# Performance work log

Measured on AMD Instinct MI355X. Metric: run time of the kernel, lower is better.

## Reference

```python
import jax, jax.numpy as jnp
import numpy as np

N, E, IN, OUT, EF = 20000, 100000, 32, 32, 16
NEG = -1e30  # finite sentinel for masked scores (avoids inf*0 grads)


def setup_inputs() -> dict:
    key = jax.random.key(0)
    ks = jax.random.split(key, 8)
    return {
        "feat": jax.random.normal(ks[0], (N, IN), jnp.float32),
        "efeat": jax.random.normal(ks[1], (E, EF), jnp.float32),
        "src": jax.random.randint(ks[2], (E,), 0, N, dtype=jnp.int32),
        "dst": jax.random.randint(ks[3], (E,), 0, N, dtype=jnp.int32),
        "etype": jax.random.randint(ks[4], (E,), 0, 2, dtype=jnp.int32),
        "attn_w": jax.random.normal(ks[5], (2 * IN, 1), jnp.float32) * 0.1,
        "attn_b": jnp.zeros((1,), jnp.float32),
        "ef1_w": jax.random.normal(ks[6], (EF, IN * OUT), jnp.float32) * 0.05,
        "ef1_b": jnp.zeros((IN * OUT,), jnp.float32),
        "ef2_w": jax.random.normal(ks[7], (EF, IN * OUT), jnp.float32) * 0.05,
        "ef2_b": jnp.zeros((IN * OUT,), jnp.float32),
        "bias": jnp.zeros((OUT,), jnp.float32),
    }


def reference(feat, efeat, src, dst, etype, attn_w, attn_b,
              ef1_w, ef1_b, ef2_w, ef2_b, bias):
    n_nodes = feat.shape[0]
    z_src = feat[src]                      # [E, IN] gather src features
    z_dst = feat[dst]                      # [E, IN] gather dst features
    # per-edge scalar attention score: leaky_relu(Linear(cat(z_src, z_dst)))
    score = jax.nn.leaky_relu(
        (jnp.concatenate([z_src, z_dst], axis=1) @ attn_w + attn_b)[:, 0]
    )  # [E]

    def relation_agg(mask, w, b):
        # edge-specific weight matrices: [E, IN, OUT]
        We = (efeat @ w + b).reshape(E, IN, OUT)
        # message per edge = src_feat @ W_e  (sum over IN commutes with attn)
        msg = jnp.einsum('ei,eio->eo', z_src, We)        # [E, OUT]
        # segment softmax over incoming edges of this relation per dst node
        s = jnp.where(mask, score, NEG)
        smax = jax.ops.segment_max(s, dst, num_segments=n_nodes)
        ex = jnp.where(mask, jnp.exp(s - smax[dst]), 0.0)
        den = jax.ops.segment_sum(ex, dst, num_segments=n_nodes)
        alpha = ex / jnp.where(den > 0, den, 1.0)[dst]   # [E]
        # attention-weighted scatter-sum to dst nodes
        return jax.ops.segment_sum(alpha[:, None] * msg, dst,
                                   num_segments=n_nodes)  # [N, OUT]

    rst = relation_agg(etype == 0, ef1_w, ef1_b) \
        + relation_agg(etype == 1, ef2_w, ef2_b) \
        + bias
    return rst
```

## Files before the change

### kernel.cpp

```cpp
#include <hip/hip_runtime.h>

typedef __attribute__((ext_vector_type(8))) short bf16x8;
typedef __attribute__((ext_vector_type(16))) float f32x16;
typedef __attribute__((ext_vector_type(2))) float f32x2;

__device__ __forceinline__ unsigned short f2b(float x) {
    unsigned u = __float_as_uint(x);
    unsigned r = (u + 0x7fffu + ((u >> 16) & 1u)) >> 16;
    return (unsigned short)r;
}
__device__ __forceinline__ unsigned f2b2(float lo, float hi) {
    return (unsigned)f2b(lo) | ((unsigned)f2b(hi) << 16);
}
__device__ __forceinline__ float b2f(unsigned short u) {
    return __uint_as_float((unsigned)u << 16);
}
__device__ __forceinline__ f32x2 pk_fma(f32x2 a, f32x2 b, f32x2 c) {
    f32x2 d;
    asm("v_pk_fma_f32 %0, %1, %2, %3" : "=v"(d) : "v"(a), "v"(b), "v"(c));
    return d;
}

__global__ void k_zero(int* __restrict__ histden, int* __restrict__ lkb,
                       const float* __restrict__ feat, const float* __restrict__ attn_w,
                       const float* __restrict__ w1, const float* __restrict__ b1,
                       const float* __restrict__ w2, const float* __restrict__ b2,
                       float* __restrict__ ps, float* __restrict__ pd,
                       unsigned short* __restrict__ PA, int N) {
    int idx = blockIdx.x * blockDim.x + threadIdx.x;
    int n4q = N;
    if (idx < n4q) ((int4*)histden)[idx] = make_int4(0, 0, 0, 0);
    if (idx < 16) ((int4*)lkb)[idx] = make_int4(0, 0, 0, 0);
    if (idx < N) {
        const float4* zp = (const float4*)(feat + (long)idx * 32);
        const float4* aw = (const float4*)attn_w;
        float a = 0.f, b = 0.f;
        #pragma unroll
        for (int j = 0; j < 8; ++j) {
            float4 z = zp[j], wa = aw[j], wb = aw[8 + j];
            a = fmaf(z.x, wa.x, a); a = fmaf(z.y, wa.y, a);
            a = fmaf(z.z, wa.z, a); a = fmaf(z.w, wa.w, a);
            b = fmaf(z.x, wb.x, b); b = fmaf(z.y, wb.y, b);
            b = fmaf(z.z, wb.z, b); b = fmaf(z.w, wb.w, b);
        }
        ps[idx] = a; pd[idx] = b;
    }
    if (idx < 2 * 17 * 2 * 64) {
        int l = idx & 63;
        int x = idx >> 6;
        int h = x & 1; x >>= 1;
        int t = x % 17;
        int r = x / 17;
        const float* W = r ? w2 : w1;
        const float* B = r ? b2 : b1;
        int o = l & 31;
        int kb = h * 16 + (l >> 5) * 8;
        unsigned short v[8];
        #pragma unroll
        for (int j = 0; j < 8; ++j) {
            int i = kb + j;
            float sv = (t < 16) ? W[t * 1024 + i * 32 + o] : B[i * 32 + o];
            v[j] = f2b(sv);
        }
        uint4 pack;
        pack.x = (unsigned)v[0] | ((unsigned)v[1] << 16);
        pack.y = (unsigned)v[2] | ((unsigned)v[3] << 16);
        pack.z = (unsigned)v[4] | ((unsigned)v[5] << 16);
        pack.w = (unsigned)v[6] | ((unsigned)v[7] << 16);
        *((uint4*)PA + idx) = pack;
    }
}

__global__ void k_hist(const int* __restrict__ dst, const int* __restrict__ etype,
                       int* __restrict__ hist, int E, int N) {
    int e = blockIdx.x * blockDim.x + threadIdx.x;
    if (e < E) atomicAdd(&hist[etype[e] * N + dst[e]], 1);
}

__global__ __launch_bounds__(256) void k_scan(const int* __restrict__ hist,
                                              int* __restrict__ rowptr,
                                              int* __restrict__ cursor,
                                              int* __restrict__ lkb, int n, int E) {
    __shared__ int s[256];
    __shared__ int soff;
    int t = threadIdx.x, b = blockIdx.x;
    int i0 = b * 1024 + t * 4;
    int4 hv = make_int4(0, 0, 0, 0);
    if (i0 + 3 < n) hv = *(const int4*)(hist + i0);
    else {
        if (i0 + 0 < n) hv.x = hist[i0 + 0];
        if (i0 + 1 < n) hv.y = hist[i0 + 1];
        if (i0 + 2 < n) hv.z = hist[i0 + 2];
        if (i0 + 3 < n) hv.w = hist[i0 + 3];
    }
    int tot = hv.x + hv.y + hv.z + hv.w;
    s[t] = tot;
    __syncthreads();
    for (int d = 1; d < 256; d <<= 1) {
        int x = (t >= d) ? s[t - d] : 0;
        __syncthreads();
        s[t] += x;
        __syncthreads();
    }
    if (t == 255) atomicExch(&lkb[b], s[255] + 1);
    if (t < 64) {
        int v = 0;
        if (t < b) {
            int p;
            do { p = atomicAdd(&lkb[t], 0); } while (p == 0);
            v = p - 1;
        }
        #pragma unroll
        for (int d = 32; d >= 1; d >>= 1) v += __shfl_down(v, d);
        if (t == 0) soff = v;
    }
    __syncthreads();
    int run = s[t] - tot + soff;
    if (i0 + 0 < n) { rowptr[i0 + 0] = run; cursor[i0 + 0] = run; } run += hv.x;
    if (i0 + 1 < n) { rowptr[i0 + 1] = run; cursor[i0 + 1] = run; } run += hv.y;
    if (i0 + 2 < n) { rowptr[i0 + 2] = run; cursor[i0 + 2] = run; } run += hv.z;
    if (i0 + 3 < n) { rowptr[i0 + 3] = run; cursor[i0 + 3] = run; }
    if (t == 0 && b == 0) rowptr[n] = E;
}

__global__ void k_score(const int* __restrict__ src, const int* __restrict__ dst,
                        const int* __restrict__ etype,
                        const float* __restrict__ ps, const float* __restrict__ pd,
                        const float* __restrict__ attn_b,
                        int* __restrict__ cursor, float* __restrict__ den,
                        int* __restrict__ sortidx, float* __restrict__ exs,
                        int E, int N) {
    int e = blockIdx.x * blockDim.x + threadIdx.x;
    if (e >= E) return;
    int d = dst[e];
    float sc = ps[src[e]] + pd[d] + attn_b[0];
    sc = sc >= 0.f ? sc : 0.01f * sc;
    float v = __expf(sc);
    int key = etype[e] * N + d;
    atomicAdd(&den[key], v);
    int pos = atomicAdd(&cursor[key], 1);
    sortidx[pos] = e;
    exs[pos] = v;
}

__global__ __launch_bounds__(256) void k_msg(
    const float* __restrict__ feat, const float* __restrict__ efeat,
    const int* __restrict__ src, const unsigned short* __restrict__ PA,
    const int* __restrict__ sortidx, const int* __restrict__ rowptr,
    unsigned short* __restrict__ wmsg, int E, int N) {
    int r = blockIdx.y;
    int cnt0 = rowptr[N];
    int relstart = r ? cnt0 : 0;
    int count = r ? (E - cnt0) : cnt0;
    int base = blockIdx.x * 128;
    if (count <= 0 || base >= count) return;

    __shared__ __align__(16) char smem[18432];
    unsigned short (*z_bf)[32] = (unsigned short(*)[32])smem;
    float (*ut)[128] = (float(*)[128])(smem + 8192);
    float (*msgl)[36] = (float(*)[36])smem;

    int tid = threadIdx.x;
    {
        int el = tid >> 1, half = tid & 1;
        int gi = base + el;
        int e = sortidx[relstart + min(gi, count - 1)];
        int sn = src[e];
        const float4* zp = (const float4*)(feat + (long)sn * 32 + half * 16);
        float4 a0 = zp[0], a1 = zp[1], a2 = zp[2], a3 = zp[3];
        uint4 p0, p1;
        p0.x = f2b2(a0.x, a0.y); p0.y = f2b2(a0.z, a0.w);
        p0.z = f2b2(a1.x, a1.y); p0.w = f2b2(a1.z, a1.w);
        p1.x = f2b2(a2.x, a2.y); p1.y = f2b2(a2.z, a2.w);
        p1.z = f2b2(a3.x, a3.y); p1.w = f2b2(a3.z, a3.w);
        uint4* zd = (uint4*)&z_bf[el][half * 16];
        zd[0] = p0; zd[1] = p1;
        const float4* up = (const float4*)(efeat + (long)e * 16 + half * 8);
        float4 c0 = up[0], c1 = up[1];
        int fb = half * 8;
        ut[fb + 0][el] = c0.x; ut[fb + 1][el] = c0.y;
        ut[fb + 2][el] = c0.z; ut[fb + 3][el] = c0.w;
        ut[fb + 4][el] = c1.x; ut[fb + 5][el] = c1.y;
        ut[fb + 6][el] = c1.z; ut[fb + 7][el] = c1.w;
    }
    __syncthreads();

    int lane = tid & 63;
    int ecol = (tid >> 6) * 32 + (lane & 31);
    int kb = (lane >> 5) * 8;
    bf16x8 b0 = *(const bf16x8*)&z_bf[ecol][kb];
    bf16x8 b1 = *(const bf16x8*)&z_bf[ecol][16 + kb];

    float uu[16];
    #pragma unroll
    for (int t = 0; t < 16; ++t) uu[t] = ut[t][ecol];

    const bf16x8* pa = (const bf16x8*)PA + (long)r * 34 * 64 + lane;

    f32x2 m2[8];
    {
        bf16x8 a0 = pa[32 * 64];
        bf16x8 a1 = pa[33 * 64];
        f32x16 c;
        #pragma unroll
        for (int k = 0; k < 16; ++k) c[k] = 0.f;
        c = __builtin_amdgcn_mfma_f32_32x32x16_bf16(a0, b0, c, 0, 0, 0);
        c = __builtin_amdgcn_mfma_f32_32x32x16_bf16(a1, b1, c, 0, 0, 0);
        #pragma unroll
        for (int k = 0; k < 8; ++k) { m2[k][0] = c[2 * k]; m2[k][1] = c[2 * k + 1]; }
    }
    #pragma unroll 4
    for (int t = 0; t < 16; ++t) {
        bf16x8 a0 = pa[(t * 2 + 0) * 64];
        bf16x8 a1 = pa[(t * 2 + 1) * 64];
        f32x16 c;
        #pragma unroll
        for (int k = 0; k < 16; ++k) c[k] = 0.f;
        c = __builtin_amdgcn_mfma_f32_32x32x16_bf16(a0, b0, c, 0, 0, 0);
        c = __builtin_amdgcn_mfma_f32_32x32x16_bf16(a1, b1, c, 0, 0, 0);
        f32x2 ud; ud[0] = uu[t]; ud[1] = uu[t];
        #pragma unroll
        for (int k = 0; k < 8; ++k) {
            f32x2 cc; cc[0] = c[2 * k]; cc[1] = c[2 * k + 1];
            m2[k] = pk_fma(ud, cc, m2[k]);
        }
    }
    __syncthreads();

    {
        int ob = 4 * (lane >> 5);
        float4* mq = (float4*)&msgl[ecol][ob];
        mq[0] = make_float4(m2[0][0], m2[0][1], m2[1][0], m2[1][1]);
        mq[2] = make_float4(m2[2][0], m2[2][1], m2[3][0], m2[3][1]);
        mq[4] = make_float4(m2[4][0], m2[4][1], m2[5][0], m2[5][1]);
        mq[6] = make_float4(m2[6][0], m2[6][1], m2[7][0], m2[7][1]);
    }
    __syncthreads();

    {
        uint4* wb = (uint4*)(wmsg + (long)(relstart + base) * 32);
        #pragma unroll
        for (int j = 0; j < 2; ++j) {
            int flat = j * 256 + tid;
            int row = flat >> 2, col = (flat & 3) * 8;
            if (base + row < count) {
                const float* mr = &msgl[row][col];
                uint4 pk;
                pk.x = f2b2(mr[0], mr[1]);
                pk.y = f2b2(mr[2], mr[3]);
                pk.z = f2b2(mr[4], mr[5]);
                pk.w = f2b2(mr[6], mr[7]);
                wb[flat] = pk;
            }
        }
    }
}

__global__ void k_reduce(const int* __restrict__ rowptr, const float* __restrict__ exs,
                         const float* __restrict__ den,
                         const unsigned short* __restrict__ wmsg,
                         const float* __restrict__ bias,
                         float* __restrict__ out, int N) {
    int tid = blockIdx.x * blockDim.x + threadIdx.x;
    if (tid >= N * 8) return;
    int n = tid >> 3, og = tid & 7;
    float4 acc = ((const float4*)bias)[og];
    #pragma unroll 1
    for (int r = 0; r < 2; ++r) {
        int k = r * N + n;
        int s = rowptr[k], e2 = rowptr[k + 1];
        if (s >= e2) continue;
        float inv = 1.f / den[k];
        #pragma unroll 1
        for (int p = s; p < e2; ++p) {
            float w = exs[p] * inv;
            ushort4 m = *(const ushort4*)(wmsg + (long)p * 32 + og * 4);
            acc.x = fmaf(w, b2f(m.x), acc.x);
            acc.y = fmaf(w, b2f(m.y), acc.y);
            acc.z = fmaf(w, b2f(m.z), acc.z);
            acc.w = fmaf(w, b2f(m.w), acc.w);
        }
    }
    ((float4*)out)[tid] = acc;
}

extern "C" void kernel_launch(void* const* d_in, const int* in_sizes, int n_in,
                              void* d_out, int out_size, void* d_ws, size_t ws_size,
                              hipStream_t stream) {
    const float* feat   = (const float*)d_in[0];
    const float* efeat  = (const float*)d_in[1];
    const int*   src    = (const int*)d_in[2];
    const int*   dst    = (const int*)d_in[3];
    const int*   etype  = (const int*)d_in[4];
    const float* attn_w = (const float*)d_in[5];
    const float* attn_b = (const float*)d_in[6];
    const float* ef1_w  = (const float*)d_in[7];
    const float* ef1_b  = (const float*)d_in[8];
    const float* ef2_w  = (const float*)d_in[9];
    const float* ef2_b  = (const float*)d_in[10];
    const float* bias   = (const float*)d_in[11];

    int E = in_sizes[2];
    int N = in_sizes[0] / 32;
    int n2 = 2 * N;
    int nb = (n2 + 1023) / 1024;

    float*          ps      = (float*)d_ws;
    float*          pd      = ps + N;
    unsigned short* PA      = (unsigned short*)(pd + N);
    int*            hist    = (int*)(PA + 2 * 17 * 2 * 64 * 8);
    float*          den     = (float*)(hist + n2);
    int*            rowptr  = (int*)(den + n2);
    int*            cursor  = rowptr + n2 + 1;
    int*            lkb     = cursor + n2;
    int*            sortidx = lkb + 64;
    float*          exs     = (float*)(sortidx + E);
    unsigned short* wmsg    = (unsigned short*)(((size_t)(exs + E) + 15) & ~(size_t)15);
    float*          out     = (float*)d_out;

    k_zero<<<(N + 255) / 256, 256, 0, stream>>>(hist, lkb, feat, attn_w,
                                                ef1_w, ef1_b, ef2_w, ef2_b,
                                                ps, pd, PA, N);
    k_hist<<<(E + 255) / 256, 256, 0, stream>>>(dst, etype, hist, E, N);
    k_scan<<<nb, 256, 0, stream>>>(hist, rowptr, cursor, lkb, n2, E);
    k_score<<<(E + 255) / 256, 256, 0, stream>>>(src, dst, etype, ps, pd, attn_b,
                                                 cursor, den, sortidx, exs, E, N);
    dim3 mgrid((E + 127) / 128, 2);
    k_msg<<<mgrid, 256, 0, stream>>>(feat, efeat, src, PA, sortidx, rowptr,
                                     wmsg, E, N);
    k_reduce<<<(N * 8 + 255) / 256, 256, 0, stream>>>(rowptr, exs, den, wmsg, bias, out, N);
}
```

Measured before the change: 52.98 us.

## Drop denominator atomics and LDS staging in message kernel

Removes the per-edge atomicAdd into the softmax denominator array. Instead, k_reduce sums the sorted exp values over each CSR segment before normalising, which costs an extra pass over exs per node. k_msg now loads each edge's source features and edge features directly into registers in MFMA operand layout and writes bf16 messages straight to global memory. This drops the LDS staging, the transposes and the three barriers, at the cost of redundant per-lane global loads and narrower, less coalesced stores. Zeroing now covers only the histogram, since the den buffer is gone.

```diff
diff --git a/kernel.cpp b/kernel.cpp
--- a/kernel.cpp
+++ b/kernel.cpp
@@ -21,15 +21,15 @@
     return d;
 }
 
-__global__ void k_zero(int* __restrict__ histden, int* __restrict__ lkb,
+__global__ void k_zero(int* __restrict__ hist, int* __restrict__ lkb,
                        const float* __restrict__ feat, const float* __restrict__ attn_w,
                        const float* __restrict__ w1, const float* __restrict__ b1,
                        const float* __restrict__ w2, const float* __restrict__ b2,
                        float* __restrict__ ps, float* __restrict__ pd,
                        unsigned short* __restrict__ PA, int N) {
     int idx = blockIdx.x * blockDim.x + threadIdx.x;
-    int n4q = N;
-    if (idx < n4q) ((int4*)histden)[idx] = make_int4(0, 0, 0, 0);
+    int n2q = (2 * N + 3) >> 2;
+    if (idx < n2q) ((int4*)hist)[idx] = make_int4(0, 0, 0, 0);
     if (idx < 16) ((int4*)lkb)[idx] = make_int4(0, 0, 0, 0);
     if (idx < N) {
         const float4* zp = (const float4*)(feat + (long)idx * 32);
@@ -127,9 +127,8 @@
                         const int* __restrict__ etype,
                         const float* __restrict__ ps, const float* __restrict__ pd,
                         const float* __restrict__ attn_b,
-                        int* __restrict__ cursor, float* __restrict__ den,
-                        int* __restrict__ sortidx, float* __restrict__ exs,
-                        int E, int N) {
+                        int* __restrict__ cursor, int* __restrict__ sortidx,
+                        float* __restrict__ exs, int E, int N) {
     int e = blockIdx.x * blockDim.x + threadIdx.x;
     if (e >= E) return;
     int d = dst[e];
@@ -137,7 +136,6 @@
     sc = sc >= 0.f ? sc : 0.01f * sc;
     float v = __expf(sc);
     int key = etype[e] * N + d;
-    atomicAdd(&den[key], v);
     int pos = atomicAdd(&cursor[key], 1);
     sortidx[pos] = e;
     exs[pos] = v;
@@ -155,45 +153,29 @@
     int base = blockIdx.x * 128;
     if (count <= 0 || base >= count) return;
 
-    __shared__ __align__(16) char smem[18432];
-    unsigned short (*z_bf)[32] = (unsigned short(*)[32])smem;
-    float (*ut)[128] = (float(*)[128])(smem + 8192);
-    float (*msgl)[36] = (float(*)[36])smem;
-
     int tid = threadIdx.x;
-    {
-        int el = tid >> 1, half = tid & 1;
-        int gi = base + el;
-        int e = sortidx[relstart + min(gi, count - 1)];
-        int sn = src[e];
-        const float4* zp = (const float4*)(feat + (long)sn * 32 + half * 16);
-        float4 a0 = zp[0], a1 = zp[1], a2 = zp[2], a3 = zp[3];
-        uint4 p0, p1;
-        p0.x = f2b2(a0.x, a0.y); p0.y = f2b2(a0.z, a0.w);
-        p0.z = f2b2(a1.x, a1.y); p0.w = f2b2(a1.z, a1.w);
-        p1.x = f2b2(a2.x, a2.y); p1.y = f2b2(a2.z, a2.w);
-        p1.z = f2b2(a3.x, a3.y); p1.w = f2b2(a3.z, a3.w);
-        uint4* zd = (uint4*)&z_bf[el][half * 16];
-        zd[0] = p0; zd[1] = p1;
-        const float4* up = (const float4*)(efeat + (long)e * 16 + half * 8);
-        float4 c0 = up[0], c1 = up[1];
-        int fb = half * 8;
-        ut[fb + 0][el] = c0.x; ut[fb + 1][el] = c0.y;
-        ut[fb + 2][el] = c0.z; ut[fb + 3][el] = c0.w;
-        ut[fb + 4][el] = c1.x; ut[fb + 5][el] = c1.y;
-        ut[fb + 6][el] = c1.z; ut[fb + 7][el] = c1.w;
-    }
-    __syncthreads();
-
     int lane = tid & 63;
     int ecol = (tid >> 6) * 32 + (lane & 31);
     int kb = (lane >> 5) * 8;
-    bf16x8 b0 = *(const bf16x8*)&z_bf[ecol][kb];
-    bf16x8 b1 = *(const bf16x8*)&z_bf[ecol][16 + kb];
-
-    float uu[16];
-    #pragma unroll
-    for (int t = 0; t < 16; ++t) uu[t] = ut[t][ecol];
+    int gi = base + ecol;
+    bool valid = gi < count;
+    int e = sortidx[relstart + min(gi, count - 1)];
+    int sn = src[e];
+
+    const float4* zp = (const float4*)(feat + (long)sn * 32);
+    float4 z0 = zp[kb >> 2], z1 = zp[(kb >> 2) + 1];
+    float4 z2 = zp[(kb >> 2) + 4], z3 = zp[(kb >> 2) + 5];
+    uint4 pb0, pb1;
+    pb0.x = f2b2(z0.x, z0.y); pb0.y = f2b2(z0.z, z0.w);
+    pb0.z = f2b2(z1.x, z1.y); pb0.w = f2b2(z1.z, z1.w);
+    pb1.x = f2b2(z2.x, z2.y); pb1.y = f2b2(z2.z, z2.w);
+    pb1.z = f2b2(z3.x, z3.y); pb1.w = f2b2(z3.z, z3.w);
+    bf16x8 b0 = *(bf16x8*)&pb0, b1 = *(bf16x8*)&pb1;
+
+    const float4* up = (const float4*)(efeat + (long)e * 16);
+    float4 u0 = up[0], u1 = up[1], u2 = up[2], u3 = up[3];
+    float uu[16] = { u0.x, u0.y, u0.z, u0.w, u1.x, u1.y, u1.z, u1.w,
+                     u2.x, u2.y, u2.z, u2.w, u3.x, u3.y, u3.z, u3.w };
 
     const bf16x8* pa = (const bf16x8*)PA + (long)r * 34 * 64 + lane;
 
@@ -225,39 +207,17 @@
             m2[k] = pk_fma(ud, cc, m2[k]);
         }
     }
-    __syncthreads();
-
-    {
-        int ob = 4 * (lane >> 5);
-        float4* mq = (float4*)&msgl[ecol][ob];
-        mq[0] = make_float4(m2[0][0], m2[0][1], m2[1][0], m2[1][1]);
-        mq[2] = make_float4(m2[2][0], m2[2][1], m2[3][0], m2[3][1]);
-        mq[4] = make_float4(m2[4][0], m2[4][1], m2[5][0], m2[5][1]);
-        mq[6] = make_float4(m2[6][0], m2[6][1], m2[7][0], m2[7][1]);
-    }
-    __syncthreads();
-
-    {
-        uint4* wb = (uint4*)(wmsg + (long)(relstart + base) * 32);
-        #pragma unroll
-        for (int j = 0; j < 2; ++j) {
-            int flat = j * 256 + tid;
-            int row = flat >> 2, col = (flat & 3) * 8;
-            if (base + row < count) {
-                const float* mr = &msgl[row][col];
-                uint4 pk;
-                pk.x = f2b2(mr[0], mr[1]);
-                pk.y = f2b2(mr[2], mr[3]);
-                pk.z = f2b2(mr[4], mr[5]);
-                pk.w = f2b2(mr[6], mr[7]);
-                wb[flat] = pk;
-            }
-        }
+
+    if (valid) {
+        unsigned short* wr = wmsg + (long)(relstart + gi) * 32 + kb / 2;
+        *(uint2*)(wr +  0) = make_uint2(f2b2(m2[0][0], m2[0][1]), f2b2(m2[1][0], m2[1][1]));
+        *(uint2*)(wr +  8) = make_uint2(f2b2(m2[2][0], m2[2][1]), f2b2(m2[3][0], m2[3][1]));
+        *(uint2*)(wr + 16) = make_uint2(f2b2(m2[4][0], m2[4][1]), f2b2(m2[5][0], m2[5][1]));
+        *(uint2*)(wr + 24) = make_uint2(f2b2(m2[6][0], m2[6][1]), f2b2(m2[7][0], m2[7][1]));
     }
 }
 
 __global__ void k_reduce(const int* __restrict__ rowptr, const float* __restrict__ exs,
-                         const float* __restrict__ den,
                          const unsigned short* __restrict__ wmsg,
                          const float* __restrict__ bias,
                          float* __restrict__ out, int N) {
@@ -270,7 +230,10 @@
         int k = r * N + n;
         int s = rowptr[k], e2 = rowptr[k + 1];
         if (s >= e2) continue;
-        float inv = 1.f / den[k];
+        float den = 0.f;
+        #pragma unroll 1
+        for (int p = s; p < e2; ++p) den += exs[p];
+        float inv = 1.f / den;
         #pragma unroll 1
         for (int p = s; p < e2; ++p) {
             float w = exs[p] * inv;
@@ -309,8 +272,7 @@
     float*          pd      = ps + N;
     unsigned short* PA      = (unsigned short*)(pd + N);
     int*            hist    = (int*)(PA + 2 * 17 * 2 * 64 * 8);
-    float*          den     = (float*)(hist + n2);
-    int*            rowptr  = (int*)(den + n2);
+    int*            rowptr  = hist + n2;
     int*            cursor  = rowptr + n2 + 1;
     int*            lkb     = cursor + n2;
     int*            sortidx = lkb + 64;
@@ -324,9 +286,9 @@
     k_hist<<<(E + 255) / 256, 256, 0, stream>>>(dst, etype, hist, E, N);
     k_scan<<<nb, 256, 0, stream>>>(hist, rowptr, cursor, lkb, n2, E);
     k_score<<<(E + 255) / 256, 256, 0, stream>>>(src, dst, etype, ps, pd, attn_b,
-                                                 cursor, den, sortidx, exs, E, N);
+                                                 cursor, sortidx, exs, E, N);
     dim3 mgrid((E + 127) / 128, 2);
     k_msg<<<mgrid, 256, 0, stream>>>(feat, efeat, src, PA, sortidx, rowptr,
                                      wmsg, E, N);
-    k_reduce<<<(N * 8 + 255) / 256, 256, 0, stream>>>(rowptr, exs, den, wmsg, bias, out, N);
-}
+    k_reduce<<<(N * 8 + 255) / 256, 256, 0, stream>>>(rowptr, exs, wmsg, bias, out, N);
+}
```

After: 50.23 us. 1.05x faster.
